# Performance work log

Hardware: AMD Instinct MI355X
Metric: run time of the kernel (lower is better)

The kernel has to match this reference:

```python
import jax, jax.numpy as jnp
import numpy as np

EPS = 1e-5  # torch InstanceNorm2d default eps


def _unfold3x3(x):
    # x: [B, C, H, W] -> [B, C, 9, H, W] (3x3 patches, zero pad=1, stride=1)
    B, C, H, W = x.shape
    xp = jnp.pad(x, ((0, 0), (0, 0), (1, 1), (1, 1)))
    return jnp.stack([xp[:, :, i:i + H, j:j + W]
                      for i in range(3) for j in range(3)], axis=2)


def _instance_norm(x):
    # InstanceNorm2d(affine=False): per-(sample, channel) spatial normalization
    m = x.mean(axis=(2, 3), keepdims=True)
    v = x.var(axis=(2, 3), keepdims=True)
    return (x - m) * jax.lax.rsqrt(v + EPS)


def setup_inputs() -> dict:
    key = jax.random.key(0)
    k1, k2, k3, k4, k5 = jax.random.split(key, 5)
    B, C, O, H, W = 8, 256, 128, 64, 64
    feat = jax.random.normal(k1, (B, C, H, W), dtype=jnp.float32)
    # scale guide so the Gaussian adaptive kernel exp(-0.5*||dg||^2) over 256
    # channels is non-degenerate (not ~delta at center)
    guide = jax.random.normal(k2, (B, C, H, W), dtype=jnp.float32) * 0.05
    pac_w = jax.random.normal(k3, (C, C, 3, 3), dtype=jnp.float32) * 0.02
    dec_w = jax.random.normal(k4, (O, C, 3, 3), dtype=jnp.float32) * 0.02
    dec_b = jax.random.normal(k5, (O,), dtype=jnp.float32) * 0.02
    return {"feat": feat, "guide": guide, "pac_w": pac_w,
            "dec_w": dec_w, "dec_b": dec_b}


def reference(feat, guide, pac_w, dec_w, dec_b):
    # --- PacConv2d: pixel-adaptive conv with fixed Gaussian guide kernel ---
    gu = _unfold3x3(guide)                      # [B,Cg,9,H,W]
    dg = gu - guide[:, :, None]                 # diff to center pixel
    kern = jnp.exp(-0.5 * jnp.sum(dg * dg, axis=1, keepdims=True))  # [B,1,9,H,W]
    xu = _unfold3x3(feat)                       # [B,C,9,H,W]
    O = pac_w.shape[0]
    pac_out = jnp.einsum('bckhw,ock->bohw', xu * kern,
                         pac_w.reshape(O, -1, 9))  # [B,C,H,W]
    # --- InstanceNorm + ReLU ---
    feat2 = jax.nn.relu(_instance_norm(pac_out))
    # --- decoding: Conv2d(3x3, pad=1) + InstanceNorm + ReLU ---
    y = jax.lax.conv_general_dilated(feat2, dec_w, window_strides=(1, 1),
                                     padding='SAME')
    y = y + dec_b[None, :, None, None]
    return jax.nn.relu(_instance_norm(y))
```

## Files before the change

### kernel.cpp

```cpp
#include <hip/hip_runtime.h>
#include <hip/hip_bf16.h>

#define IN_EPS 1e-5f

typedef __attribute__((ext_vector_type(8))) short short8;
typedef __attribute__((ext_vector_type(4))) float f32x4;

__device__ __forceinline__ short f2bf(float f) {
  __hip_bfloat16 h = (__hip_bfloat16)f;
  return *(short*)&h;
}
__device__ __forceinline__ float bf2f(short s) {
  union { unsigned u; float f; } x;
  x.u = ((unsigned)(unsigned short)s) << 16;
  return x.f;
}

__global__ void wconv_k(const float* __restrict__ src, short* __restrict__ dst,
                        int O) {
  int idx = blockIdx.x * 256 + threadIdx.x;
  if (idx >= O * 2304) return;
  int o = idx / 2304;
  int r = idx - o * 2304;
  int c = r / 9;
  int k = r - c * 9;
  int mblk = o >> 7, ol = o & 127, cb = c >> 6, cl = c & 63;
  dst[(((size_t)(mblk * 36 + cb * 9 + k)) << 13) + (ol << 6) + (cl ^ ((ol & 7) << 3))]
      = f2bf(src[idx]);
}

__global__ __launch_bounds__(256) void kern_k(const float* __restrict__ g,
                                              float* __restrict__ kern) {
  int h = blockIdx.x, b = blockIdx.y;
  int t = threadIdx.x, w = t & 63, cg = t >> 6;
  float acc[9];
#pragma unroll
  for (int k = 0; k < 9; ++k) acc[k] = 0.f;
  const float* base = g + (((size_t)b * 256 + (cg << 6)) << 12) + (h << 6) + w;
#pragma unroll 4
  for (int cc = 0; cc < 64; ++cc) {
    const float* gp = base + ((size_t)cc << 12);
    float mid = gp[0];
    float top = (h > 0) ? gp[-64] : 0.f;
    float bot = (h < 63) ? gp[64] : 0.f;
    float rows[3] = {top, mid, bot};
#pragma unroll
    for (int i = 0; i < 3; ++i) {
      float v = rows[i];
      float l = __shfl_up(v, 1);
      float r = __shfl_down(v, 1);
      if (w == 0) l = 0.f;
      if (w == 63) r = 0.f;
      float dl = l - mid, dm = v - mid, dr = r - mid;
      acc[i * 3 + 0] += dl * dl;
      acc[i * 3 + 1] += dm * dm;
      acc[i * 3 + 2] += dr * dr;
    }
  }
  __shared__ float red[4][9][64];
#pragma unroll
  for (int k = 0; k < 9; ++k) red[cg][k][w] = acc[k];
  __syncthreads();
  for (int idx = t; idx < 576; idx += 256) {
    int k = idx >> 6, w2 = idx & 63;
    float s = red[0][k][w2] + red[1][k][w2] + red[2][k][w2] + red[3][k][w2];
    kern[(((size_t)b * 9 + k) << 12) + (h << 6) + w2] = expf(-0.5f * s);
  }
}

template <int MBLKS, int BN, bool USE_KERN, bool USE_NORM>
__global__ __launch_bounds__(512, 4) void gemm_conv(
    const short* __restrict__ Wimg, const float* __restrict__ X,
    const float* __restrict__ Kf, const float* __restrict__ MRin,
    float* __restrict__ out) {
  constexpr int MOUT = MBLKS * 128;
  constexpr int ROWS = BN / 64;
  constexpr int HR = ROWS + 2;
  constexpr int WN = BN / 4;
  constexpr int NF = BN / 64;
  __shared__ short ldsA[8192];
  __shared__ short ldsB[HR * 64 * 64];
  __shared__ short ldsS[HR * 2 * 64];
  __shared__ float klds[USE_KERN ? 9 * BN : 1];

  const int t = threadIdx.x;
  const int nblk = blockIdx.x, mblk = blockIdx.y, b = blockIdx.z;
  const int h0 = nblk * ROWS;
  const int lane = t & 63, wid = t >> 6;
  const int wr = wid >> 2, wc = wid & 3;
  const int fr = lane & 15, kg = (lane >> 4) << 3;
  const int scol = t & 63;
  const int c8 = (t >> 6) << 3;

  f32x4 acc[4][NF];
#pragma unroll
  for (int i = 0; i < 4; ++i)
#pragma unroll
    for (int j = 0; j < NF; ++j) acc[i][j] = {0.f, 0.f, 0.f, 0.f};

  float breg[HR][8];
  float2 mreg[8];

  auto loadA = [&](int step, short8* ar) {
    const short* src = Wimg + (((size_t)(mblk * 36 + step)) << 13) + (t << 3);
    ar[0] = *(const short8*)(src);
    ar[1] = *(const short8*)(src + 4096);
  };
  auto writeA = [&](const short8* ar) {
    *(short8*)&ldsA[t << 3] = ar[0];
    *(short8*)&ldsA[4096 + (t << 3)] = ar[1];
  };
  auto loadBregs = [&](int cbn) {
    int c0 = cbn << 6;
    const float* base = X + (((size_t)b * 256 + c0 + c8) << 12) + scol;
    if (USE_NORM) {
#pragma unroll
      for (int i = 0; i < 8; ++i)
        mreg[i] = ((const float2*)MRin)[b * 256 + c0 + c8 + i];
    }
#pragma unroll
    for (int r = 0; r < HR; ++r) {
      int hr = h0 - 1 + r;
      bool okr = (unsigned)hr < 64u;
      const float* src = base + (hr << 6);
#pragma unroll
      for (int i = 0; i < 8; ++i)
        breg[r][i] = okr ? src[(size_t)i << 12] : 0.f;
    }
  };
  auto writeB = [&]() {
#pragma unroll
    for (int r = 0; r < HR; ++r) {
      short8 pk;
#pragma unroll
      for (int i = 0; i < 8; ++i) {
        float x = breg[r][i];
        if (USE_NORM) x = fmaxf((x - mreg[i].x) * mreg[i].y, 0.f);
        pk[i] = f2bf(x);
      }
      *(short8*)&ldsB[(((r << 6) + scol) << 6) + (c8 ^ ((scol & 7) << 3))] = pk;
    }
  };
  auto computeTap = [&](int tap) {
    const int di = tap / 3 - 1, dj = tap % 3 - 1;
    float kfv[NF];
    if (USE_KERN) {
#pragma unroll
      for (int nf = 0; nf < NF; ++nf)
        kfv[nf] = klds[tap * BN + wc * WN + (nf << 4) + fr];
    }
#pragma unroll
    for (int ks = 0; ks < 2; ++ks) {
      int kb = (ks << 5) + kg;
      short8 a4[4], b2[NF];
#pragma unroll
      for (int mf = 0; mf < 4; ++mf) {
        int rr = (wr << 6) + (mf << 4) + fr;
        a4[mf] = *(const short8*)&ldsA[(rr << 6) + (kb ^ ((rr & 7) << 3))];
      }
#pragma unroll
      for (int nf = 0; nf < NF; ++nf) {
        int px = wc * WN + (nf << 4) + fr;
        int rr2 = (px >> 6) + di + 1;
        int wcol = (px & 63) + dj;
        int kbs = kb ^ ((wcol & 7) << 3);
        const short* pm = &ldsB[(((rr2 << 6) + wcol) << 6) + kbs];
        const short* ps = &ldsS[(((rr2 << 1) + (wcol == 64)) << 6) + kbs];
        short8 bb = *(const short8*)(((unsigned)wcol < 64u) ? pm : ps);
        if (USE_KERN) {
#pragma unroll
          for (int i = 0; i < 8; ++i) bb[i] = f2bf(bf2f(bb[i]) * kfv[nf]);
        }
        b2[nf] = bb;
      }
#pragma unroll
      for (int mf = 0; mf < 4; ++mf)
#pragma unroll
        for (int nf = 0; nf < NF; ++nf)
          acc[mf][nf] = __builtin_amdgcn_mfma_f32_16x16x32_bf16(
              a4[mf], b2[nf], acc[mf][nf], 0, 0, 0);
    }
  };

  if (t < HR * 16) {
    short8 z = {0, 0, 0, 0, 0, 0, 0, 0};
    *(short8*)&ldsS[t << 3] = z;
  }
  if (USE_KERN) {
    for (int idx = t; idx < 9 * BN; idx += 512) {
      int tap = idx / BN, px = idx & (BN - 1);
      klds[idx] = Kf[(((size_t)b * 9 + tap) << 12) +
                     ((h0 + (px >> 6)) << 6) + (px & 63)];
    }
  }
  {
    short8 ar[2];
    loadA(0, ar);
    loadBregs(0);
    writeA(ar);
    writeB();
  }
  __syncthreads();

  int cb = 0, tap = 0;
  for (int step = 0; step < 36; ++step) {
    bool more = (step + 1) < 36;
    bool lastTap = (tap == 8);
    short8 ar[2];
    if (more) loadA(step + 1, ar);
    if (more && lastTap) loadBregs(cb + 1);
    computeTap(tap);
    __syncthreads();
    if (more) {
      writeA(ar);
      if (lastTap) writeB();
      __syncthreads();
    }
    if (++tap == 9) { tap = 0; ++cb; }
  }

  const int row4 = (lane >> 4) << 2;
#pragma unroll
  for (int mf = 0; mf < 4; ++mf) {
    int o = (mblk << 7) + (wr << 6) + (mf << 4) + row4;
    size_t ob = (((size_t)b * MOUT + o) << 12) + nblk * BN + wc * WN + fr;
#pragma unroll
    for (int nf = 0; nf < NF; ++nf) {
      f32x4 v = acc[mf][nf];
      size_t oo = ob + (nf << 4);
      out[oo] = v[0];
      out[oo + 4096] = v[1];
      out[oo + 8192] = v[2];
      out[oo + 12288] = v[3];
    }
  }
}

__global__ __launch_bounds__(256) void reduce_mv(const float* __restrict__ x,
                                                 float* __restrict__ mr) {
  int bc = blockIdx.x, t = threadIdx.x;
  const float4* xp = (const float4*)(x + ((size_t)bc << 12));
  float s = 0.f, s2 = 0.f;
  for (int i = t; i < 1024; i += 256) {
    float4 v = xp[i];
    s += v.x + v.y + v.z + v.w;
    s2 += v.x * v.x + v.y * v.y + v.z * v.z + v.w * v.w;
  }
#pragma unroll
  for (int off = 32; off; off >>= 1) {
    s += __shfl_down(s, off);
    s2 += __shfl_down(s2, off);
  }
  __shared__ float ls[4], ls2[4];
  int wid = t >> 6, lane = t & 63;
  if (!lane) { ls[wid] = s; ls2[wid] = s2; }
  __syncthreads();
  if (!t) {
    s = ls[0] + ls[1] + ls[2] + ls[3];
    s2 = ls2[0] + ls2[1] + ls2[2] + ls2[3];
    float m = s * (1.f / 4096.f);
    float var = s2 * (1.f / 4096.f) - m * m;
    mr[2 * bc] = m;
    mr[2 * bc + 1] = rsqrtf(fmaxf(var, 0.f) + IN_EPS);
  }
}

__global__ __launch_bounds__(256) void finalize_k(const float* __restrict__ y,
                                                  const float* __restrict__ mr,
                                                  float* __restrict__ out) {
  int i = blockIdx.x * 256 + threadIdx.x;
  int bc = i >> 10;
  float m = mr[2 * bc], r = mr[2 * bc + 1];
  float4 v = ((const float4*)y)[i];
  v.x = fmaxf((v.x - m) * r, 0.f);
  v.y = fmaxf((v.y - m) * r, 0.f);
  v.z = fmaxf((v.z - m) * r, 0.f);
  v.w = fmaxf((v.w - m) * r, 0.f);
  ((float4*)out)[i] = v;
}

extern "C" void kernel_launch(void* const* d_in, const int* in_sizes, int n_in,
                              void* d_out, int out_size, void* d_ws,
                              size_t ws_size, hipStream_t stream) {
  (void)in_sizes; (void)n_in; (void)out_size; (void)ws_size;
  const float* feat  = (const float*)d_in[0];
  const float* guide = (const float*)d_in[1];
  const float* pac_w = (const float*)d_in[2];
  const float* dec_w = (const float*)d_in[3];
  float* out = (float*)d_out;
  char* ws = (char*)d_ws;

  float* kernbuf = (float*)(ws);
  short* Ws1     = (short*)(ws + 0x120000);
  short* Ws2     = (short*)(ws + 0x240000);
  float* mr1     = (float*)(ws + 0x2D0000);
  float* mr2     = (float*)(ws + 0x2D4000);
  float* pac     = (float*)(ws + 0x300000);
  float* ybuf    = (float*)(ws + 0x2300000);

  wconv_k<<<(256 * 2304 + 255) / 256, 256, 0, stream>>>(pac_w, Ws1, 256);
  wconv_k<<<(128 * 2304 + 255) / 256, 256, 0, stream>>>(dec_w, Ws2, 128);
  kern_k<<<dim3(64, 8), 256, 0, stream>>>(guide, kernbuf);

  gemm_conv<2, 128, true, false><<<dim3(32, 2, 8), 512, 0, stream>>>(
      Ws1, feat, kernbuf, nullptr, pac);
  reduce_mv<<<8 * 256, 256, 0, stream>>>(pac, mr1);
  gemm_conv<1, 64, false, true><<<dim3(64, 1, 8), 512, 0, stream>>>(
      Ws2, pac, nullptr, mr1, ybuf);
  reduce_mv<<<8 * 128, 256, 0, stream>>>(ybuf, mr2);
  finalize_k<<<4096, 256, 0, stream>>>(ybuf, mr2, out);
}
```

Before: 149.6 us.

## Double-buffer weights via direct global-to-LDS loads and apply guide kernel post-MFMA

Weight tiles now go straight into a double-buffered LDS array through global_load_lds, which removes the register round trip and one barrier per step. The per-pixel Gaussian kernel is no longer multiplied into each bf16 B operand before the MFMA. Each tap instead accumulates into a partial tile that is scaled by the kernel value and added to the accumulator, which saves the per-element conversions but costs extra registers and FMAs. Both GEMMs are fixed at a 128-pixel N tile with MFMA priority raised, so the decoder conv runs with half as many blocks.

```diff
diff --git a/kernel.cpp b/kernel.cpp
--- a/kernel.cpp
+++ b/kernel.cpp
@@ -10,10 +10,11 @@
   __hip_bfloat16 h = (__hip_bfloat16)f;
   return *(short*)&h;
 }
-__device__ __forceinline__ float bf2f(short s) {
-  union { unsigned u; float f; } x;
-  x.u = ((unsigned)(unsigned short)s) << 16;
-  return x.f;
+
+__device__ __forceinline__ void glds16(const void* g, void* l) {
+  typedef const __attribute__((address_space(1))) void gconst_t;
+  typedef __attribute__((address_space(3))) void lds_t;
+  __builtin_amdgcn_global_load_lds((gconst_t*)g, (lds_t*)l, 16, 0, 0);
 }
 
 __global__ void wconv_k(const float* __restrict__ src, short* __restrict__ dst,
@@ -68,47 +69,41 @@
   }
 }
 
-template <int MBLKS, int BN, bool USE_KERN, bool USE_NORM>
+template <int MBLKS, bool USE_KERN, bool USE_NORM>
 __global__ __launch_bounds__(512, 4) void gemm_conv(
     const short* __restrict__ Wimg, const float* __restrict__ X,
     const float* __restrict__ Kf, const float* __restrict__ MRin,
     float* __restrict__ out) {
   constexpr int MOUT = MBLKS * 128;
-  constexpr int ROWS = BN / 64;
-  constexpr int HR = ROWS + 2;
-  constexpr int WN = BN / 4;
-  constexpr int NF = BN / 64;
-  __shared__ short ldsA[8192];
-  __shared__ short ldsB[HR * 64 * 64];
-  __shared__ short ldsS[HR * 2 * 64];
-  __shared__ float klds[USE_KERN ? 9 * BN : 1];
+  __shared__ short ldsA[2][8192];
+  __shared__ short ldsB[4 * 64 * 64];
+  __shared__ short ldsS[4 * 2 * 64];
+  __shared__ float klds[USE_KERN ? 9 * 128 : 1];
 
   const int t = threadIdx.x;
   const int nblk = blockIdx.x, mblk = blockIdx.y, b = blockIdx.z;
-  const int h0 = nblk * ROWS;
+  const int h0 = nblk * 2;
   const int lane = t & 63, wid = t >> 6;
   const int wr = wid >> 2, wc = wid & 3;
   const int fr = lane & 15, kg = (lane >> 4) << 3;
   const int scol = t & 63;
   const int c8 = (t >> 6) << 3;
 
-  f32x4 acc[4][NF];
+  f32x4 acc[4][2];
 #pragma unroll
   for (int i = 0; i < 4; ++i)
 #pragma unroll
-    for (int j = 0; j < NF; ++j) acc[i][j] = {0.f, 0.f, 0.f, 0.f};
-
-  float breg[HR][8];
+    for (int j = 0; j < 2; ++j) acc[i][j] = {0.f, 0.f, 0.f, 0.f};
+
+  float breg[4][8];
   float2 mreg[8];
 
-  auto loadA = [&](int step, short8* ar) {
-    const short* src = Wimg + (((size_t)(mblk * 36 + step)) << 13) + (t << 3);
-    ar[0] = *(const short8*)(src);
-    ar[1] = *(const short8*)(src + 4096);
-  };
-  auto writeA = [&](const short8* ar) {
-    *(short8*)&ldsA[t << 3] = ar[0];
-    *(short8*)&ldsA[4096 + (t << 3)] = ar[1];
+  auto stageA = [&](int step, int buf) {
+    const short* src = Wimg + (((size_t)(mblk * 36 + step)) << 13);
+#pragma unroll
+    for (int i = 0; i < 2; ++i)
+      glds16(src + (((i << 9) + t) << 3),
+             &ldsA[buf][((i << 9) + (wid << 6)) << 3]);
   };
   auto loadBregs = [&](int cbn) {
     int c0 = cbn << 6;
@@ -119,7 +114,7 @@
         mreg[i] = ((const float2*)MRin)[b * 256 + c0 + c8 + i];
     }
 #pragma unroll
-    for (int r = 0; r < HR; ++r) {
+    for (int r = 0; r < 4; ++r) {
       int hr = h0 - 1 + r;
       bool okr = (unsigned)hr < 64u;
       const float* src = base + (hr << 6);
@@ -130,7 +125,7 @@
   };
   auto writeB = [&]() {
 #pragma unroll
-    for (int r = 0; r < HR; ++r) {
+    for (int r = 0; r < 4; ++r) {
       short8 pk;
 #pragma unroll
       for (int i = 0; i < 8; ++i) {
@@ -141,81 +136,87 @@
       *(short8*)&ldsB[(((r << 6) + scol) << 6) + (c8 ^ ((scol & 7) << 3))] = pk;
     }
   };
-  auto computeTap = [&](int tap) {
+  auto computeTap = [&](int tap, int buf) {
+    const short* As = ldsA[buf];
     const int di = tap / 3 - 1, dj = tap % 3 - 1;
-    float kfv[NF];
+    f32x4 part[4][2];
     if (USE_KERN) {
 #pragma unroll
-      for (int nf = 0; nf < NF; ++nf)
-        kfv[nf] = klds[tap * BN + wc * WN + (nf << 4) + fr];
-    }
+      for (int i = 0; i < 4; ++i)
+#pragma unroll
+        for (int j = 0; j < 2; ++j) part[i][j] = {0.f, 0.f, 0.f, 0.f};
+    }
+    f32x4(&dst)[4][2] = *(USE_KERN ? &part : &acc);
 #pragma unroll
     for (int ks = 0; ks < 2; ++ks) {
       int kb = (ks << 5) + kg;
-      short8 a4[4], b2[NF];
+      short8 a4[4], b2[2];
 #pragma unroll
       for (int mf = 0; mf < 4; ++mf) {
         int rr = (wr << 6) + (mf << 4) + fr;
-        a4[mf] = *(const short8*)&ldsA[(rr << 6) + (kb ^ ((rr & 7) << 3))];
+        a4[mf] = *(const short8*)&As[(rr << 6) + (kb ^ ((rr & 7) << 3))];
       }
 #pragma unroll
-      for (int nf = 0; nf < NF; ++nf) {
-        int px = wc * WN + (nf << 4) + fr;
+      for (int nf = 0; nf < 2; ++nf) {
+        int px = (wc << 5) + (nf << 4) + fr;
         int rr2 = (px >> 6) + di + 1;
         int wcol = (px & 63) + dj;
         int kbs = kb ^ ((wcol & 7) << 3);
         const short* pm = &ldsB[(((rr2 << 6) + wcol) << 6) + kbs];
         const short* ps = &ldsS[(((rr2 << 1) + (wcol == 64)) << 6) + kbs];
-        short8 bb = *(const short8*)(((unsigned)wcol < 64u) ? pm : ps);
-        if (USE_KERN) {
-#pragma unroll
-          for (int i = 0; i < 8; ++i) bb[i] = f2bf(bf2f(bb[i]) * kfv[nf]);
+        b2[nf] = *(const short8*)(((unsigned)wcol < 64u) ? pm : ps);
+      }
+      __builtin_amdgcn_s_setprio(1);
+#pragma unroll
+      for (int mf = 0; mf < 4; ++mf)
+#pragma unroll
+        for (int nf = 0; nf < 2; ++nf)
+          dst[mf][nf] = __builtin_amdgcn_mfma_f32_16x16x32_bf16(
+              a4[mf], b2[nf], dst[mf][nf], 0, 0, 0);
+      __builtin_amdgcn_s_setprio(0);
+    }
+    if (USE_KERN) {
+      float kq0 = klds[tap * 128 + (wc << 5) + fr];
+      float kq1 = klds[tap * 128 + (wc << 5) + 16 + fr];
+#pragma unroll
+      for (int mf = 0; mf < 4; ++mf)
+#pragma unroll
+        for (int j = 0; j < 4; ++j) {
+          acc[mf][0][j] += kq0 * part[mf][0][j];
+          acc[mf][1][j] += kq1 * part[mf][1][j];
         }
-        b2[nf] = bb;
-      }
-#pragma unroll
-      for (int mf = 0; mf < 4; ++mf)
-#pragma unroll
-        for (int nf = 0; nf < NF; ++nf)
-          acc[mf][nf] = __builtin_amdgcn_mfma_f32_16x16x32_bf16(
-              a4[mf], b2[nf], acc[mf][nf], 0, 0, 0);
     }
   };
 
-  if (t < HR * 16) {
+  if (t < 64) {
     short8 z = {0, 0, 0, 0, 0, 0, 0, 0};
     *(short8*)&ldsS[t << 3] = z;
   }
   if (USE_KERN) {
-    for (int idx = t; idx < 9 * BN; idx += 512) {
-      int tap = idx / BN, px = idx & (BN - 1);
+    for (int idx = t; idx < 1152; idx += 512) {
+      int tap = idx >> 7, px = idx & 127;
       klds[idx] = Kf[(((size_t)b * 9 + tap) << 12) +
                      ((h0 + (px >> 6)) << 6) + (px & 63)];
     }
   }
-  {
-    short8 ar[2];
-    loadA(0, ar);
-    loadBregs(0);
-    writeA(ar);
-    writeB();
-  }
+  stageA(0, 0);
+  loadBregs(0);
+  writeB();
   __syncthreads();
 
   int cb = 0, tap = 0;
   for (int step = 0; step < 36; ++step) {
+    int cur = step & 1, nxt = cur ^ 1;
     bool more = (step + 1) < 36;
     bool lastTap = (tap == 8);
-    short8 ar[2];
-    if (more) loadA(step + 1, ar);
+    if (more) stageA(step + 1, nxt);
     if (more && lastTap) loadBregs(cb + 1);
-    computeTap(tap);
+    computeTap(tap, cur);
+    if (more && lastTap) {
+      __syncthreads();
+      writeB();
+    }
     __syncthreads();
-    if (more) {
-      writeA(ar);
-      if (lastTap) writeB();
-      __syncthreads();
-    }
     if (++tap == 9) { tap = 0; ++cb; }
   }
 
@@ -223,9 +224,9 @@
 #pragma unroll
   for (int mf = 0; mf < 4; ++mf) {
     int o = (mblk << 7) + (wr << 6) + (mf << 4) + row4;
-    size_t ob = (((size_t)b * MOUT + o) << 12) + nblk * BN + wc * WN + fr;
-#pragma unroll
-    for (int nf = 0; nf < NF; ++nf) {
+    size_t ob = (((size_t)b * MOUT + o) << 12) + (nblk << 7) + (wc << 5) + fr;
+#pragma unroll
+    for (int nf = 0; nf < 2; ++nf) {
       f32x4 v = acc[mf][nf];
       size_t oo = ob + (nf << 4);
       out[oo] = v[0];
@@ -302,10 +303,10 @@
   wconv_k<<<(128 * 2304 + 255) / 256, 256, 0, stream>>>(dec_w, Ws2, 128);
   kern_k<<<dim3(64, 8), 256, 0, stream>>>(guide, kernbuf);
 
-  gemm_conv<2, 128, true, false><<<dim3(32, 2, 8), 512, 0, stream>>>(
+  gemm_conv<2, true, false><<<dim3(32, 2, 8), 512, 0, stream>>>(
       Ws1, feat, kernbuf, nullptr, pac);
   reduce_mv<<<8 * 256, 256, 0, stream>>>(pac, mr1);
-  gemm_conv<1, 64, false, true><<<dim3(64, 1, 8), 512, 0, stream>>>(
+  gemm_conv<1, false, true><<<dim3(32, 1, 8), 512, 0, stream>>>(
       Ws2, pac, nullptr, mr1, ybuf);
   reduce_mv<<<8 * 128, 256, 0, stream>>>(ybuf, mr2);
   finalize_k<<<4096, 256, 0, stream>>>(ybuf, mr2, out);
```

Result: slower. 175.0 us (+17.0%).
